# Kernel optimization log

Hardware: AMD Instinct MI355X
Metric: run time of the kernel (lower is better)

Reference implementation:

```python
import jax, jax.numpy as jnp
from jax import lax
import numpy as np

K = 32          # PyG radius_graph default max_num_neighbors
NEG = -1e9      # mask fill for max-aggregation


def _gather(a, i):  # a [N,C], i [...,] int -> a[i]
    return a[i]


def radius_knn(pos, r):
    # pos [B,N,3] -> (idx [B,N,K], valid [B,N,K]) nearest-K within radius r, self excluded
    sq = jnp.sum(pos * pos, -1)                                   # [B,N]
    d2 = sq[:, :, None] + sq[:, None, :] - 2.0 * jnp.einsum('bnc,bmc->bnm', pos, pos)
    N = pos.shape[1]
    d2 = d2 + jnp.eye(N, dtype=pos.dtype) * 1e9                    # exclude self-loops
    neg, idx = lax.top_k(-d2, K)
    valid = (-neg) <= r * r
    return idx, valid


def fps(pos, n):
    # iterative farthest point sampling, deterministic start at index 0; pos [B,N,3] -> idx [B,n]
    def one(p):
        mind0 = jnp.sum((p - p[0]) ** 2, -1)
        def step(mind, _):
            i = jnp.argmax(mind)
            nd = jnp.sum((p - p[i]) ** 2, -1)
            return jnp.minimum(mind, nd), i
        _, idxs = lax.scan(step, mind0, None, length=n - 1)
        return jnp.concatenate([jnp.zeros((1,), jnp.int32), idxs.astype(jnp.int32)])
    return jax.vmap(one)(pos)


def point_conv(x, pos, idx, valid, W1, b1, W2, b2):
    # PyG PointNetConv: msg = local_nn(concat(x_j, pos_j - pos_i)), max-aggregate
    g = jax.vmap(_gather)
    rel = g(pos, idx) - pos[:, :, None, :]                         # [B,N,K,3]
    feat = rel if x is None else jnp.concatenate([g(x, idx), rel], -1)
    h = jax.nn.relu(feat @ W1 + b1) @ W2 + b2                      # [B,N,K,C]
    h = jnp.where(valid[..., None], h, NEG)
    return jnp.max(h, axis=2)                                      # [B,N,C]


def _forward(pos, W1a, b1a, W1b, b1b, W2a, b2a, W2b, b2b, W3a, b3a, W3b, b3b,
             Wc1, bc1, Wc2, bc2, Wc3, bc3, Wd1, bd1, Wd2, bd2):
    take = jax.vmap(_gather)
    B, N, _ = pos.shape
    idx, v = radius_knn(pos, 0.2)
    x = jax.nn.relu(point_conv(None, pos, idx, v, W1a, b1a, W1b, b1b))
    fi = fps(pos, N // 2)
    x, pos = take(x, fi), take(pos, fi)
    idx, v = radius_knn(pos, 0.4)
    x = jax.nn.relu(point_conv(x, pos, idx, v, W2a, b2a, W2b, b2b))
    fi = fps(pos, N // 8)
    x, pos = take(x, fi), take(pos, fi)
    idx, v = radius_knn(pos, 1.0)
    x = jax.nn.relu(point_conv(x, pos, idx, v, W3a, b3a, W3b, b3b))
    feat = jnp.max(x, axis=1)                                      # global max pool [B,256]
    h = jax.nn.relu(feat @ Wc1 + bc1)
    h = jax.nn.relu(h @ Wc2 + bc2)                                 # dropout is identity in eval
    logits = h @ Wc3 + bc3
    h2 = jax.nn.relu(feat @ Wd1 + bd1)
    d = h2 @ Wd2 + bd2
    return jax.nn.log_softmax(logits, axis=-1), jax.nn.log_softmax(d, axis=-1)


def setup_inputs() -> dict:
    key = jax.random.key(0)
    ks = jax.random.split(key, 32)
    def lin(k, fin, fout):
        kw, kb = jax.random.split(k)
        s = 1.0 / np.sqrt(fin)
        return (jax.random.uniform(kw, (fin, fout), jnp.float32, -s, s),
                jax.random.uniform(kb, (fout,), jnp.float32, -s, s))
    inp = {'pos': jax.random.uniform(ks[0], (8, 4096, 3), jnp.float32)}
    names = [('W1a','b1a',3,64),('W1b','b1b',64,64),('W2a','b2a',67,128),('W2b','b2b',128,128),
             ('W3a','b3a',131,256),('W3b','b3b',256,256),('Wc1','bc1',256,256),('Wc2','bc2',256,256),
             ('Wc3','bc3',256,40),('Wd1','bd1',256,256),('Wd2','bd2',256,2)]
    for i, (wn, bn, fin, fout) in enumerate(names):
        W, b = lin(ks[i + 1], fin, fout)
        inp[wn], inp[bn] = W, b
    return inp


def reference(pos, W1a, b1a, W1b, b1b, W2a, b2a, W2b, b2b, W3a, b3a, W3b, b3b,
              Wc1, bc1, Wc2, bc2, Wc3, bc3, Wd1, bd1, Wd2, bd2):
    return _forward(pos, W1a, b1a, W1b, b1b, W2a, b2a, W2b, b2b, W3a, b3a, W3b, b3b,
                    Wc1, bc1, Wc2, bc2, Wc3, bc3, Wd1, bd1, Wd2, bd2)
```

## Files before the change

### kernel.cpp

```cpp
#include <hip/hip_runtime.h>


#define NB 8

__device__ __forceinline__ unsigned obits(float f) {
  unsigned u = __float_as_uint(f);
  return (u & 0x80000000u) ? ~u : (u | 0x80000000u);
}

static constexpr int CAND = 1024;

template<int CTRL>
__device__ __forceinline__ unsigned long long dpp_max_step(unsigned long long v) {
  const int lo = (int)(unsigned)(v & 0xffffffffull);
  const int hi = (int)(unsigned)(v >> 32);
  const unsigned nlo = (unsigned)__builtin_amdgcn_update_dpp(lo, lo, CTRL, 0xf, 0xf, false);
  const unsigned nhi = (unsigned)__builtin_amdgcn_update_dpp(hi, hi, CTRL, 0xf, 0xf, false);
  const unsigned long long nv = ((unsigned long long)nhi << 32) | nlo;
  return (nv > v) ? nv : v;
}

__device__ __forceinline__ unsigned wave_iscan_add(unsigned x) {
  x += (unsigned)__builtin_amdgcn_update_dpp(0, (int)x, 0x111, 0xf, 0xf, true);
  x += (unsigned)__builtin_amdgcn_update_dpp(0, (int)x, 0x112, 0xf, 0xf, true);
  x += (unsigned)__builtin_amdgcn_update_dpp(0, (int)x, 0x114, 0xf, 0xf, true);
  x += (unsigned)__builtin_amdgcn_update_dpp(0, (int)x, 0x118, 0xf, 0xf, true);
  x += (unsigned)__builtin_amdgcn_update_dpp(0, (int)x, 0x142, 0xa, 0xf, true);
  x += (unsigned)__builtin_amdgcn_update_dpp(0, (int)x, 0x143, 0xc, 0xf, true);
  return x;
}

__device__ __forceinline__ unsigned long long u64max(unsigned long long a,
                                                    unsigned long long b) {
  return (b > a) ? b : a;
}

__device__ __forceinline__ void set_wave_prio_hi() {
#if __has_builtin(__builtin_amdgcn_s_setprio)
  __builtin_amdgcn_s_setprio(3);
#endif
}

template<int N, int NOUT, int T>
__device__ __forceinline__ void fps_body(char* sm, const float* __restrict__ pb,
                                         int* __restrict__ fi, int b) {
  constexpr int P = N / T;
  constexpr int NW = T / 64;
  constexpr int CELLS = (N >= 4096) ? 512 : 256;
  constexpr int CZB = (CELLS == 512) ? 3 : 2;
  constexpr int CH = NOUT;
  constexpr int NCHUNK = N / CH;
  static_assert(CH % P == 0 && N % CH == 0, "chunking");
  int4* sPosI = (int4*)sm;
  int*  sfi   = (int*)(sm + (size_t)N * 16);
  unsigned long long* sKey =
      (unsigned long long*)(sm + (size_t)N * 16 + NOUT * 4);
  unsigned* hist = (unsigned*)(sm + (size_t)N * 16 + NOUT * 4 + 128);
  int* sOrd = sfi;
  const int tid = threadIdx.x, wid = tid >> 6, lane = tid & 63;
  set_wave_prio_hi();

  for (int t = tid; t < N; t += T) {
    sPosI[t] = make_int4((int)(pb[3*t]   * 8388608.f),
                         (int)(pb[3*t+1] * 8388608.f),
                         (int)(pb[3*t+2] * 8388608.f), 0);
  }
  for (int c = tid; c < CELLS; c += T) hist[c] = 0u;
  __syncthreads();

  unsigned myc[P];
#pragma unroll
  for (int r = 0; r < P; r++) {
    const int t = tid + r * T;
    const int4 p4 = sPosI[t];
    const unsigned cell = (((unsigned)p4.x >> 20) << (3 + CZB)) |
                          (((unsigned)p4.y >> 20) << CZB) |
                          ((unsigned)p4.z >> (23 - CZB));
    myc[r] = cell;
    atomicAdd(&hist[cell], 1u);
  }
  __syncthreads();

  {
    unsigned* sPart = (unsigned*)sKey;
    unsigned v = (tid < CELLS) ? hist[tid] : 0u;
    const unsigned isc = wave_iscan_add(v);
    if (lane == 63) sPart[wid] = isc;
    __syncthreads();
    unsigned offs = 0;
#pragma unroll
    for (int w2 = 0; w2 < NW; w2++) offs += (w2 < wid) ? sPart[w2] : 0u;
    if (tid < CELLS) hist[tid] = offs + isc - v;
    __syncthreads();
  }

  int myslot[P];
#pragma unroll
  for (int r = 0; r < P; r++) myslot[r] = (int)atomicAdd(&hist[myc[r]], 1u);

  int ex[P], ey[P], ez[P]; unsigned einv[P];
  for (int pc = 0; pc < NCHUNK; pc++) {
    __syncthreads();
#pragma unroll
    for (int r = 0; r < P; r++) {
      const int s = myslot[r];
      if (s >= pc * CH && s < (pc + 1) * CH) sOrd[s - pc * CH] = tid + r * T;
    }
    __syncthreads();
    if ((tid * P) / CH == pc) {
#pragma unroll
      for (int e = 0; e < P; e++) {
        const int o = sOrd[tid * P + e - pc * CH];
        const int4 p4 = sPosI[o];
        ex[e] = p4.x; ey[e] = p4.y; ez[e] = p4.z;
        einv[e] = (unsigned)(4095 - o);
      }
    }
  }
  __syncthreads();

  int lox = ex[0], hix = ex[0], loy = ey[0], hiy = ey[0], loz = ez[0], hiz = ez[0];
#pragma unroll
  for (int e = 1; e < P; e++) {
    lox = min(lox, ex[e]); hix = max(hix, ex[e]);
    loy = min(loy, ey[e]); hiy = max(hiy, ey[e]);
    loz = min(loz, ez[e]); hiz = max(hiz, ez[e]);
  }

  const int4 p0 = sPosI[0];
  unsigned long long mind[P];
  unsigned long long bv;
  {
    unsigned long long tv[P];
#pragma unroll
    for (int e = 0; e < P; e++) {
      const long long dx = ex[e] - p0.x, dy = ey[e] - p0.y, dz = ez[e] - p0.z;
      const unsigned long long d2 =
          (unsigned long long)(dx * dx + dy * dy + dz * dz);
      const unsigned long long k = (d2 << 12) | einv[e];
      mind[e] = k; tv[e] = k;
    }
#pragma unroll
    for (int s = 1; s < P; s <<= 1)
#pragma unroll
      for (int e = 0; e + s < P; e += 2 * s)
        if (tv[e + s] > tv[e]) tv[e] = tv[e + s];
    bv = tv[0];
  }
  if (tid == 0) sfi[0] = 0;

  for (int t = 1; t < NOUT; t++) {
    unsigned long long v = bv;
    v = dpp_max_step<0x111>(v);
    v = dpp_max_step<0x112>(v);
    v = dpp_max_step<0x114>(v);
    v = dpp_max_step<0x118>(v);
    v = dpp_max_step<0x142>(v);
    v = dpp_max_step<0x143>(v);
    const int pp = t & 1;
    if (lane == 63) sKey[pp * NW + wid] = v;
    __syncthreads();
    unsigned long long best;
    if (NW == 8) {
      unsigned long long k0 = sKey[pp*8+0], k1 = sKey[pp*8+1],
                         k2 = sKey[pp*8+2], k3 = sKey[pp*8+3],
                         k4 = sKey[pp*8+4], k5 = sKey[pp*8+5],
                         k6 = sKey[pp*8+6], k7 = sKey[pp*8+7];
      k0 = u64max(k0, k1); k2 = u64max(k2, k3);
      k4 = u64max(k4, k5); k6 = u64max(k6, k7);
      k0 = u64max(k0, k2); k4 = u64max(k4, k6);
      best = u64max(k0, k4);
    } else {
      unsigned long long k0 = sKey[pp*NW+0];
#pragma unroll
      for (int w2 = 1; w2 < NW; w2++) k0 = u64max(k0, sKey[pp*NW+w2]);
      best = k0;
    }
    const int ii = 4095 - (int)(best & 0xFFFull);
    if (tid == 0) sfi[t] = ii;
    const int4 wc = sPosI[ii];

    const int ax = max(max(lox - wc.x, wc.x - hix), 0);
    const int ay = max(max(loy - wc.y, wc.y - hiy), 0);
    const int az = max(max(loz - wc.z, wc.z - hiz), 0);
    const unsigned long long lb =
        (unsigned long long)ax * (unsigned long long)ax +
        (unsigned long long)ay * (unsigned long long)ay +
        (unsigned long long)az * (unsigned long long)az;
    if (lb < (bv >> 12)) {
      unsigned long long tv[P];
#pragma unroll
      for (int e = 0; e < P; e++) {
        const long long dx = ex[e] - wc.x, dy = ey[e] - wc.y, dz = ez[e] - wc.z;
        const unsigned long long nd =
            (unsigned long long)(dx * dx + dy * dy + dz * dz);
        const unsigned long long nk = (nd << 12) | einv[e];
        unsigned long long mk = mind[e];
        mk = (nk < mk) ? nk : mk;
        mind[e] = mk;
        tv[e] = mk;
      }
#pragma unroll
      for (int s = 1; s < P; s <<= 1)
#pragma unroll
        for (int e = 0; e + s < P; e += 2 * s)
          if (tv[e + s] > tv[e]) tv[e] = tv[e + s];
      bv = tv[0];
    }
  }
  __syncthreads();
  for (int t = tid; t < NOUT; t += T) fi[(size_t)b * NOUT + t] = sfi[t];
}

template<int N, int H, int C, bool HASX, bool FOLDMAX, int T>
__device__ __forceinline__ void knnconv_body(
    char* sm, const float* __restrict__ pb, int b, int i,
    const float* __restrict__ U, const float* __restrict__ Wrel,
    const float* __restrict__ b1, const float* __restrict__ W2,
    const float* __restrict__ b2, float* __restrict__ out, double rr) {
  constexpr int HCHUNK = (C == 64) ? 64 : (C == 128 ? 32 : 16);
  constexpr int STR = HCHUNK + 4;
  constexpr int NW = T / 64;
  constexpr int EPK = 32 / NW;
  constexpr int BPT = 2048 / T;
  constexpr int KNNFRONT = N * 8 + 13312;
  constexpr int CONVFRONT = 32 * H * 4 + C * STR * 4;
  constexpr int FRONT = (KNNFRONT > CONVFRONT) ? KNNFRONT : CONVFRONT;
  static_assert(32 * H * 4 >= NW * C * 4, "sRed must fit inside h1s");
  double*   d2s     = (double*)sm;
  unsigned* hist    = (unsigned*)(sm + N * 8);
  int*      candIdx = (int*)(sm + N * 8 + 8192);
  unsigned* sWT     = (unsigned*)(sm + N * 8 + 12288);
  float* h1s  = (float*)sm;
  float* sW2T = (float*)(sm + 32 * H * 4);
  float* sRed = (float*)sm;
  int*   snbr = (int*)(sm + FRONT);
  float* rel  = (float*)(sm + FRONT + 128);
  int*   pcnt = (int*)(sm + FRONT + 128 + 384);
  int*   pbin = pcnt + 1;
  const int tid = threadIdx.x;

  const double xi = pb[3*i], yi = pb[3*i+1], zi = pb[3*i+2];
  const double si = (xi*xi + yi*yi) + zi*zi;
  for (int t = tid; t < 2048; t += T) hist[t] = 0u;
  if (tid == 0) *pcnt = 0;
  __syncthreads();
  for (int j = tid; j < N; j += T) {
    double xj = pb[3*j], yj = pb[3*j+1], zj = pb[3*j+2];
    double sj = (xj*xj + yj*yj) + zj*zj;
    double dt = (xi*xj + yi*yj) + zi*zj;
    double d2 = (si + sj) - 2.0*dt;
    if (j == i) d2 += 1e9;
    d2s[j] = d2;
    atomicAdd(&hist[obits((float)d2) >> 21], 1u);
  }
  __syncthreads();
  unsigned lsum = 0;
  const int base = tid * BPT;
#pragma unroll
  for (int q = 0; q < BPT; q++) lsum += hist[base + q];
  const unsigned isc = wave_iscan_add(lsum);
  if ((tid & 63) == 63) sWT[tid >> 6] = isc;
  __syncthreads();
  {
    const int wid = tid >> 6;
    unsigned offs = 0;
#pragma unroll
    for (int w2 = 0; w2 < NW; w2++) offs += (w2 < wid) ? sWT[w2] : 0u;
    const unsigned incl = isc + offs, excl = incl - lsum;
    if (excl < 32u && incl >= 32u) {
      unsigned c = excl;
      for (int q = 0; q < BPT; q++) {
        c += hist[base + q];
        if (c >= 32u) { *pbin = base + q; break; }
      }
    }
  }
  __syncthreads();
  const int binT = *pbin;
  for (int j = tid; j < N; j += T) {
    if ((int)(obits((float)d2s[j]) >> 21) <= binT) {
      int p = atomicAdd(pcnt, 1);
      if (p < CAND) candIdx[p] = j;
    }
  }
  __syncthreads();
  const int M = min(*pcnt, CAND);
  for (int c = tid; c < M; c += T) {
    const int j = candIdx[c];
    const double d = d2s[j];
    int rank = 0;
    for (int e = 0; e < M; e++) {
      const int j2 = candIdx[e];
      const double de = d2s[j2];
      rank += (de < d || (de == d && j2 < j)) ? 1 : 0;
    }
    if (rank < 32) snbr[rank] = (d <= rr) ? j : -1;
  }
  __syncthreads();

  if (tid < 32) {
    const int j = snbr[tid];
    float rx = 0.f, ry = 0.f, rz = 0.f;
    if (j >= 0) {
      rx = pb[3*j]   - pb[3*i];
      ry = pb[3*j+1] - pb[3*i+1];
      rz = pb[3*j+2] - pb[3*i+2];
    }
    rel[tid*3+0] = rx; rel[tid*3+1] = ry; rel[tid*3+2] = rz;
  }
  __syncthreads();

  constexpr int QPK = H / 4;
  for (int qi = tid; qi < 32 * QPK; qi += T) {
    const int k = qi / QPK, h0 = (qi - k * QPK) * 4;
    const int j = snbr[k];
    float4 v = make_float4(0.f, 0.f, 0.f, 0.f);
    if (j >= 0) {
      float4 a = HASX ? *(const float4*)&U[((size_t)b * N + j) * H + h0]
                      : *(const float4*)&b1[h0];
      const float rx = rel[k*3], ry = rel[k*3+1], rz = rel[k*3+2];
      const float4 w0 = *(const float4*)&Wrel[h0];
      const float4 w1 = *(const float4*)&Wrel[H + h0];
      const float4 w2 = *(const float4*)&Wrel[2 * H + h0];
      a.x += rx * w0.x + ry * w1.x + rz * w2.x;
      a.y += rx * w0.y + ry * w1.y + rz * w2.y;
      a.z += rx * w0.z + ry * w1.z + rz * w2.z;
      a.w += rx * w0.w + ry * w1.w + rz * w2.w;
      v = make_float4(fmaxf(a.x, 0.f), fmaxf(a.y, 0.f),
                      fmaxf(a.z, 0.f), fmaxf(a.w, 0.f));
    }
    *(float4*)&h1s[k * H + h0] = v;
  }
  const int cc = tid & 63;
  const int kk = tid >> 6;
  constexpr int CC = C / 64;
  float acc[EPK][CC];
#pragma unroll
  for (int e = 0; e < EPK; e++)
#pragma unroll
    for (int q = 0; q < CC; q++) acc[e][q] = 0.f;
  for (int hc = 0; hc < H; hc += HCHUNK) {
    __syncthreads();
    for (int idx = tid; idx < HCHUNK * C; idx += T) {
      const int hh = idx / C, c = idx - hh * C;
      sW2T[c * STR + hh] = W2[(size_t)(hc + hh) * C + c];
    }
    __syncthreads();
    for (int hh0 = 0; hh0 < HCHUNK; hh0 += 4) {
      float4 wv[CC];
#pragma unroll
      for (int q = 0; q < CC; q++)
        wv[q] = *(const float4*)&sW2T[(cc + q * 64) * STR + hh0];
#pragma unroll
      for (int e = 0; e < EPK; e++) {
        const float4 hv = *(const float4*)&h1s[(kk + e * NW) * H + hc + hh0];
#pragma unroll
        for (int q = 0; q < CC; q++) {
          acc[e][q] += hv.x * wv[q].x;
          acc[e][q] += hv.y * wv[q].y;
          acc[e][q] += hv.z * wv[q].z;
          acc[e][q] += hv.w * wv[q].w;
        }
      }
    }
  }
  float m[CC];
#pragma unroll
  for (int q = 0; q < CC; q++) m[q] = -1e9f;
#pragma unroll
  for (int e = 0; e < EPK; e++) {
    if (snbr[kk + e * NW] >= 0) {
#pragma unroll
      for (int q = 0; q < CC; q++) m[q] = fmaxf(m[q], acc[e][q]);
    }
  }
  __syncthreads();
#pragma unroll
  for (int q = 0; q < CC; q++) sRed[kk * C + cc + q * 64] = m[q];
  __syncthreads();
  if (kk == 0) {
#pragma unroll
    for (int q = 0; q < CC; q++) {
      const int c = cc + q * 64;
      float mm = sRed[c];
#pragma unroll
      for (int w2 = 1; w2 < NW; w2++) mm = fmaxf(mm, sRed[w2 * C + c]);
      const float o = (mm > -5e8f) ? (mm + b2[c]) : -1e9f;
      const float r = fmaxf(o, 0.f);
      if (FOLDMAX) {
        atomicMax((int*)&out[b * C + c], __float_as_int(r));
      } else {
        out[((size_t)b * N + i) * C + c] = r;
      }
    }
  }
}

template<int N, int NOUT, int H, int C, bool HASX, int SMSIZE>
__device__ __forceinline__ void stage_fused_impl(
    const float* pos, double rr, int* fi, const float* U, const float* Wrel,
    const float* b1, const float* W2, const float* b2, float* out, char* sm) {
  if (blockIdx.x < NB) {
    fps_body<N, NOUT, 512>(sm, pos + (size_t)blockIdx.x * N * 3, fi, blockIdx.x);
  } else {
    const int row = blockIdx.x - NB;
    const int b = row / N;
    const int i = row - b * N;
    knnconv_body<N, H, C, HASX, false, 512>(sm, pos + (size_t)b * N * 3, b, i,
                                            U, Wrel, b1, W2, b2, out, rr);
  }
}

__global__ __launch_bounds__(512, 2)
void stage1_kernel(const float* __restrict__ pos, double rr, int* __restrict__ fi,
                   const float* __restrict__ Wrel, const float* __restrict__ b1,
                   const float* __restrict__ W2, const float* __restrict__ b2,
                   float* __restrict__ out) {
  __shared__ __align__(16) char sm[75904];
  stage_fused_impl<4096, 2048, 64, 64, false, 75904>(
      pos, rr, fi, nullptr, Wrel, b1, W2, b2, out, sm);
}

__global__ __launch_bounds__(512, 2)
void stage2_kernel(const float* __restrict__ pos, double rr, int* __restrict__ fi,
                   const float* __restrict__ U, const float* __restrict__ Wrel,
                   const float* __restrict__ b1, const float* __restrict__ W2,
                   const float* __restrict__ b2, float* __restrict__ out) {
  __shared__ __align__(16) char sm[39440];
  stage_fused_impl<2048, 512, 128, 128, true, 39440>(
      pos, rr, fi, U, Wrel, b1, W2, b2, out, sm);
}

__global__ __launch_bounds__(512)
void stage3_kernel(const float* __restrict__ pos, double rr,
                   const float* __restrict__ U, const float* __restrict__ Wrel,
                   const float* __restrict__ b1, const float* __restrict__ W2,
                   const float* __restrict__ b2, float* __restrict__ feat) {
  __shared__ __align__(16) char sm[53776];
  const int b = blockIdx.x / 512;
  const int i = blockIdx.x - b * 512;
  knnconv_body<512, 256, 256, true, true, 512>(sm, pos + (size_t)b * 512 * 3,
                                               b, i, U, Wrel, b1, W2, b2,
                                               feat, rr);
}

template<int CIN, int HH>
__global__ __launch_bounds__(HH)
void gp_kernel(const float* __restrict__ X, const float* __restrict__ posPrev,
               const int* __restrict__ fi, int Nprev, int M,
               const float* __restrict__ W, const float* __restrict__ bias,
               float* __restrict__ U, float* __restrict__ posDst) {
  const int row = blockIdx.x;
  const int b = row / M;
  const int tid = threadIdx.x;
  const int j = fi[row];
  __shared__ float sx[CIN];
  if (tid < CIN) sx[tid] = X[((size_t)b * Nprev + j) * CIN + tid];
  if (tid < 3) posDst[(size_t)row * 3 + tid] = posPrev[((size_t)b * Nprev + j) * 3 + tid];
  __syncthreads();
  float a = bias[tid];
  for (int f = 0; f < CIN; f++) a = fmaf(sx[f], W[f * HH + tid], a);
  U[(size_t)row * HH + tid] = a;
}

__global__ __launch_bounds__(256) void head_kernel(
    const float* __restrict__ feat,
    const float* __restrict__ Wc1, const float* __restrict__ bc1,
    const float* __restrict__ Wc2, const float* __restrict__ bc2,
    const float* __restrict__ Wc3, const float* __restrict__ bc3,
    const float* __restrict__ Wd1, const float* __restrict__ bd1,
    const float* __restrict__ Wd2, const float* __restrict__ bd2,
    float* __restrict__ out) {
  const int b = blockIdx.x, tid = threadIdx.x;
  __shared__ float sf[256], sh[256], sh2[256], shd[256], sl[48];
  sf[tid] = feat[b * 256 + tid];
  __syncthreads();
  float a = bc1[tid], ad = bd1[tid];
  for (int f = 0; f < 256; f++) {
    const float fv = sf[f];
    a  = fmaf(fv, Wc1[f * 256 + tid], a);
    ad = fmaf(fv, Wd1[f * 256 + tid], ad);
  }
  sh[tid] = fmaxf(a, 0.f);
  shd[tid] = fmaxf(ad, 0.f);
  __syncthreads();
  float a2 = bc2[tid];
  for (int f = 0; f < 256; f++) a2 = fmaf(sh[f], Wc2[f * 256 + tid], a2);
  sh2[tid] = fmaxf(a2, 0.f);
  __syncthreads();
  if (tid < 40) {
    float l = bc3[tid];
    for (int f = 0; f < 256; f++) l = fmaf(sh2[f], Wc3[f * 40 + tid], l);
    sl[tid] = l;
  }
  if (tid >= 64 && tid < 66) {
    const int q = tid - 64;
    float l = bd2[q];
    for (int f = 0; f < 256; f++) l = fmaf(shd[f], Wd2[f * 2 + q], l);
    sl[40 + q] = l;
  }
  __syncthreads();
  if (tid == 0) {
    float m0 = sl[0];
    for (int q = 1; q < 40; q++) m0 = fmaxf(m0, sl[q]);
    float s = 0.f;
    for (int q = 0; q < 40; q++) s += expf(sl[q] - m0);
    const float ls = logf(s);
    for (int q = 0; q < 40; q++) out[b * 40 + q] = sl[q] - m0 - ls;
    const float m1 = fmaxf(sl[40], sl[41]);
    const float s1 = expf(sl[40] - m1) + expf(sl[41] - m1);
    const float ls1 = logf(s1);
    out[320 + b * 2 + 0] = sl[40] - m1 - ls1;
    out[320 + b * 2 + 1] = sl[41] - m1 - ls1;
  }
}

extern "C" void kernel_launch(void* const* d_in, const int* in_sizes, int n_in,
                              void* d_out, int out_size, void* d_ws, size_t ws_size,
                              hipStream_t stream) {
  (void)in_sizes; (void)n_in; (void)out_size; (void)ws_size;
  const float* pos = (const float*)d_in[0];
  const float* W1a = (const float*)d_in[1];  const float* b1a = (const float*)d_in[2];
  const float* W1b = (const float*)d_in[3];  const float* b1b = (const float*)d_in[4];
  const float* W2a = (const float*)d_in[5];  const float* b2a = (const float*)d_in[6];
  const float* W2b = (const float*)d_in[7];  const float* b2b = (const float*)d_in[8];
  const float* W3a = (const float*)d_in[9];  const float* b3a = (const float*)d_in[10];
  const float* W3b = (const float*)d_in[11]; const float* b3b = (const float*)d_in[12];
  const float* Wc1 = (const float*)d_in[13]; const float* bc1 = (const float*)d_in[14];
  const float* Wc2 = (const float*)d_in[15]; const float* bc2 = (const float*)d_in[16];
  const float* Wc3 = (const float*)d_in[17]; const float* bc3 = (const float*)d_in[18];
  const float* Wd1 = (const float*)d_in[19]; const float* bd1 = (const float*)d_in[20];
  const float* Wd2 = (const float*)d_in[21]; const float* bd2 = (const float*)d_in[22];
  float* out = (float*)d_out;

  char* w = (char*)d_ws;
  auto alloc = [&](size_t bytes) -> void* {
    void* p = (void*)w;
    w += (bytes + 255) & ~(size_t)255;
    return p;
  };
  int*   fi1  = (int*)  alloc((size_t)NB*2048*4);
  float* x1   = (float*)alloc((size_t)NB*4096*64*4);
  float* pos2 = (float*)alloc((size_t)NB*2048*3*4);
  float* U2   = (float*)alloc((size_t)NB*2048*128*4);
  float* x2   = (float*)alloc((size_t)NB*2048*128*4);
  int*   fi2  = (int*)  alloc((size_t)NB*512*4);
  float* pos3 = (float*)alloc((size_t)NB*512*3*4);
  float* U3   = (float*)alloc((size_t)NB*512*256*4);
  float* feat = (float*)alloc((size_t)NB*256*4);

  hipMemsetAsync(feat, 0, (size_t)NB * 256 * 4, stream);

  stage1_kernel<<<NB + NB * 4096, 512, 0, stream>>>(
      pos, 0.2 * 0.2, fi1, W1a, b1a, W1b, b1b, x1);

  gp_kernel<64, 128><<<NB * 2048, 128, 0, stream>>>(
      x1, pos, fi1, 4096, 2048, W2a, b2a, U2, pos2);

  stage2_kernel<<<NB + NB * 2048, 512, 0, stream>>>(
      pos2, 0.4 * 0.4, fi2, U2, W2a + (size_t)64 * 128, b2a, W2b, b2b, x2);

  gp_kernel<128, 256><<<NB * 512, 256, 0, stream>>>(
      x2, pos2, fi2, 2048, 512, W3a, b3a, U3, pos3);

  stage3_kernel<<<NB * 512, 512, 0, stream>>>(
      pos3, 1.0, U3, W3a + (size_t)128 * 256, b3a, W3b, b3b, feat);

  head_kernel<<<NB, 256, 0, stream>>>(feat, Wc1, bc1, Wc2, bc2, Wc3, bc3,
                                      Wd1, bd1, Wd2, bd2, out);
}
```

Baseline: 2.364 ms.

## Select two FPS points per barrier round when the runner-up stays valid

```diff
diff --git a/kernel.cpp b/kernel.cpp
--- a/kernel.cpp
+++ b/kernel.cpp
@@ -18,6 +18,22 @@
   const unsigned nhi = (unsigned)__builtin_amdgcn_update_dpp(hi, hi, CTRL, 0xf, 0xf, false);
   const unsigned long long nv = ((unsigned long long)nhi << 32) | nlo;
   return (nv > v) ? nv : v;
+}
+
+__device__ __forceinline__ unsigned long long wave_max_u64(unsigned long long v) {
+  v = dpp_max_step<0x111>(v);
+  v = dpp_max_step<0x112>(v);
+  v = dpp_max_step<0x114>(v);
+  v = dpp_max_step<0x118>(v);
+  v = dpp_max_step<0x142>(v);
+  v = dpp_max_step<0x143>(v);
+  return v;
+}
+
+__device__ __forceinline__ unsigned long long bcast63(unsigned long long v) {
+  const unsigned lo = (unsigned)__builtin_amdgcn_readlane((int)(unsigned)(v & 0xffffffffull), 63);
+  const unsigned hi = (unsigned)__builtin_amdgcn_readlane((int)(unsigned)(v >> 32), 63);
+  return ((unsigned long long)hi << 32) | lo;
 }
 
 __device__ __forceinline__ unsigned wave_iscan_add(unsigned x) {
@@ -51,11 +67,13 @@
   constexpr int CH = NOUT;
   constexpr int NCHUNK = N / CH;
   static_assert(CH % P == 0 && N % CH == 0, "chunking");
+  static_assert(NW == 8, "dual-selection protocol sized for 8 waves");
   int4* sPosI = (int4*)sm;
   int*  sfi   = (int*)(sm + (size_t)N * 16);
-  unsigned long long* sKey =
+  unsigned long long* sKey2 =
       (unsigned long long*)(sm + (size_t)N * 16 + NOUT * 4);
-  unsigned* hist = (unsigned*)(sm + (size_t)N * 16 + NOUT * 4 + 128);
+  int4* sPosW = (int4*)(sm + (size_t)N * 16 + NOUT * 4 + 256);
+  unsigned* hist = (unsigned*)(sm + (size_t)N * 16 + NOUT * 4 + 768);
   int* sOrd = sfi;
   const int tid = threadIdx.x, wid = tid >> 6, lane = tid & 63;
   set_wave_prio_hi();
@@ -82,7 +100,7 @@
   __syncthreads();
 
   {
-    unsigned* sPart = (unsigned*)sKey;
+    unsigned* sPart = (unsigned*)sKey2;
     unsigned v = (tid < CELLS) ? hist[tid] : 0u;
     const unsigned isc = wave_iscan_add(v);
     if (lane == 63) sPart[wid] = isc;
@@ -129,7 +147,7 @@
 
   const int4 p0 = sPosI[0];
   unsigned long long mind[P];
-  unsigned long long bv;
+  unsigned long long bv, t2loc;
   {
     unsigned long long tv[P];
 #pragma unroll
@@ -146,70 +164,121 @@
       for (int e = 0; e + s < P; e += 2 * s)
         if (tv[e + s] > tv[e]) tv[e] = tv[e + s];
     bv = tv[0];
+    unsigned long long t2 = 0;
+#pragma unroll
+    for (int e = 0; e < P; e++) t2 = (mind[e] == bv) ? t2 : u64max(t2, mind[e]);
+    t2loc = t2;
   }
   if (tid == 0) sfi[0] = 0;
 
-  for (int t = 1; t < NOUT; t++) {
-    unsigned long long v = bv;
-    v = dpp_max_step<0x111>(v);
-    v = dpp_max_step<0x112>(v);
-    v = dpp_max_step<0x114>(v);
-    v = dpp_max_step<0x118>(v);
-    v = dpp_max_step<0x142>(v);
-    v = dpp_max_step<0x143>(v);
-    const int pp = t & 1;
-    if (lane == 63) sKey[pp * NW + wid] = v;
+  int t = 1, rnd = 0;
+  while (t < NOUT) {
+    const int pp = rnd & 1; rnd++;
+    unsigned long long v = wave_max_u64(bv);
+    const unsigned long long s1 = bcast63(v);
+    unsigned long long v2 = wave_max_u64((bv == s1) ? t2loc : bv);
+    const unsigned long long s2 = bcast63(v2);
+    if (lane == 63) {
+      ulonglong2 kv; kv.x = v; kv.y = v2;
+      ((ulonglong2*)sKey2)[pp * 8 + wid] = kv;
+    }
+#pragma unroll
+    for (int e = 0; e < P; e++) {
+      if (mind[e] == s1) sPosW[pp * 16 + wid * 2 + 0] = make_int4(ex[e], ey[e], ez[e], 0);
+      if (mind[e] == s2) sPosW[pp * 16 + wid * 2 + 1] = make_int4(ex[e], ey[e], ez[e], 0);
+    }
     __syncthreads();
-    unsigned long long best;
-    if (NW == 8) {
-      unsigned long long k0 = sKey[pp*8+0], k1 = sKey[pp*8+1],
-                         k2 = sKey[pp*8+2], k3 = sKey[pp*8+3],
-                         k4 = sKey[pp*8+4], k5 = sKey[pp*8+5],
-                         k6 = sKey[pp*8+6], k7 = sKey[pp*8+7];
-      k0 = u64max(k0, k1); k2 = u64max(k2, k3);
-      k4 = u64max(k4, k5); k6 = u64max(k6, k7);
-      k0 = u64max(k0, k2); k4 = u64max(k4, k6);
-      best = u64max(k0, k4);
-    } else {
-      unsigned long long k0 = sKey[pp*NW+0];
-#pragma unroll
-      for (int w2 = 1; w2 < NW; w2++) k0 = u64max(k0, sKey[pp*NW+w2]);
-      best = k0;
-    }
-    const int ii = 4095 - (int)(best & 0xFFFull);
-    if (tid == 0) sfi[t] = ii;
-    const int4 wc = sPosI[ii];
-
-    const int ax = max(max(lox - wc.x, wc.x - hix), 0);
-    const int ay = max(max(loy - wc.y, wc.y - hiy), 0);
-    const int az = max(max(loz - wc.z, wc.z - hiz), 0);
-    const unsigned long long lb =
-        (unsigned long long)ax * (unsigned long long)ax +
-        (unsigned long long)ay * (unsigned long long)ay +
-        (unsigned long long)az * (unsigned long long)az;
-    if (lb < (bv >> 12)) {
+    ulonglong2 kw[8];
+    {
+      const ulonglong2* kk = ((const ulonglong2*)sKey2) + pp * 8;
+#pragma unroll
+      for (int w2 = 0; w2 < 8; w2++) kw[w2] = kk[w2];
+    }
+    const unsigned long long K1 =
+        u64max(u64max(u64max(kw[0].x, kw[1].x), u64max(kw[2].x, kw[3].x)),
+               u64max(u64max(kw[4].x, kw[5].x), u64max(kw[6].x, kw[7].x)));
+    unsigned long long c[8];
+#pragma unroll
+    for (int w2 = 0; w2 < 8; w2++) c[w2] = (kw[w2].x == K1) ? kw[w2].y : kw[w2].x;
+    const unsigned long long K2 =
+        u64max(u64max(u64max(c[0], c[1]), u64max(c[2], c[3])),
+               u64max(u64max(c[4], c[5]), u64max(c[6], c[7])));
+    int sA = 0, sB = 0;
+#pragma unroll
+    for (int w2 = 0; w2 < 8; w2++) {
+      if (kw[w2].x == K1) sA = w2 * 2;
+      if (kw[w2].x == K2) sB = w2 * 2;
+      if (kw[w2].y == K2) sB = w2 * 2 + 1;
+    }
+    const int4 A  = sPosW[pp * 16 + sA];
+    const int4 Bq = sPosW[pp * 16 + sB];
+    const long long dabx = A.x - Bq.x, daby = A.y - Bq.y, dabz = A.z - Bq.z;
+    const unsigned long long d2ab =
+        (unsigned long long)(dabx * dabx + daby * daby + dabz * dabz);
+    const bool canDual = (t + 1 < NOUT) && (d2ab >= (K2 >> 12));
+    if (tid == 0) {
+      sfi[t] = 4095 - (int)(K1 & 0xFFFull);
+      if (canDual) sfi[t + 1] = 4095 - (int)(K2 & 0xFFFull);
+    }
+    const unsigned long long thr = bv >> 12;
+    bool updA, updB = false;
+    {
+      const int ax = max(max(lox - A.x, A.x - hix), 0);
+      const int ay = max(max(loy - A.y, A.y - hiy), 0);
+      const int az = max(max(loz - A.z, A.z - hiz), 0);
+      const unsigned long long lb =
+          (unsigned long long)ax * (unsigned long long)ax +
+          (unsigned long long)ay * (unsigned long long)ay +
+          (unsigned long long)az * (unsigned long long)az;
+      updA = lb < thr;
+      if (updA) {
+#pragma unroll
+        for (int e = 0; e < P; e++) {
+          const long long dx = ex[e] - A.x, dy = ey[e] - A.y, dz = ez[e] - A.z;
+          const unsigned long long nk =
+              ((unsigned long long)(dx * dx + dy * dy + dz * dz) << 12) | einv[e];
+          if (nk < mind[e]) mind[e] = nk;
+        }
+      }
+    }
+    if (canDual) {
+      const int ax = max(max(lox - Bq.x, Bq.x - hix), 0);
+      const int ay = max(max(loy - Bq.y, Bq.y - hiy), 0);
+      const int az = max(max(loz - Bq.z, Bq.z - hiz), 0);
+      const unsigned long long lb =
+          (unsigned long long)ax * (unsigned long long)ax +
+          (unsigned long long)ay * (unsigned long long)ay +
+          (unsigned long long)az * (unsigned long long)az;
+      updB = lb < thr;
+      if (updB) {
+#pragma unroll
+        for (int e = 0; e < P; e++) {
+          const long long dx = ex[e] - Bq.x, dy = ey[e] - Bq.y, dz = ez[e] - Bq.z;
+          const unsigned long long nk =
+              ((unsigned long long)(dx * dx + dy * dy + dz * dz) << 12) | einv[e];
+          if (nk < mind[e]) mind[e] = nk;
+        }
+      }
+    }
+    if (updA || updB) {
       unsigned long long tv[P];
 #pragma unroll
-      for (int e = 0; e < P; e++) {
-        const long long dx = ex[e] - wc.x, dy = ey[e] - wc.y, dz = ez[e] - wc.z;
-        const unsigned long long nd =
-            (unsigned long long)(dx * dx + dy * dy + dz * dz);
-        const unsigned long long nk = (nd << 12) | einv[e];
-        unsigned long long mk = mind[e];
-        mk = (nk < mk) ? nk : mk;
-        mind[e] = mk;
-        tv[e] = mk;
-      }
+      for (int e = 0; e < P; e++) tv[e] = mind[e];
 #pragma unroll
       for (int s = 1; s < P; s <<= 1)
 #pragma unroll
         for (int e = 0; e + s < P; e += 2 * s)
           if (tv[e + s] > tv[e]) tv[e] = tv[e + s];
       bv = tv[0];
-    }
-  }
-  __syncthreads();
-  for (int t = tid; t < NOUT; t += T) fi[(size_t)b * NOUT + t] = sfi[t];
+      unsigned long long t2 = 0;
+#pragma unroll
+      for (int e = 0; e < P; e++) t2 = (mind[e] == bv) ? t2 : u64max(t2, mind[e]);
+      t2loc = t2;
+    }
+    t += canDual ? 2 : 1;
+  }
+  __syncthreads();
+  for (int t2 = tid; t2 < NOUT; t2 += T) fi[(size_t)b * NOUT + t2] = sfi[t2];
 }
 
 template<int N, int H, int C, bool HASX, bool FOLDMAX, int T>
@@ -417,8 +486,8 @@
                    const float* __restrict__ Wrel, const float* __restrict__ b1,
                    const float* __restrict__ W2, const float* __restrict__ b2,
                    float* __restrict__ out) {
-  __shared__ __align__(16) char sm[75904];
-  stage_fused_impl<4096, 2048, 64, 64, false, 75904>(
+  __shared__ __align__(16) char sm[76544];
+  stage_fused_impl<4096, 2048, 64, 64, false, 76544>(
       pos, rr, fi, nullptr, Wrel, b1, W2, b2, out, sm);
 }
 
```

Measured after the change: 3.458 ms. 1.46x slower.
